# Kernel tuning notes

Measured on AMD Instinct MI355X. Metric: run time of the kernel, lower is better.

Reference implementation:

```python
import jax, jax.numpy as jnp
import numpy as np

E_LAMBDA = 1e-4


def _conv1d(x, w, b=None, pad=0):
    # x: (C, L) unbatched, w: (O, I, K)
    y = jax.lax.conv_general_dilated(
        x[None], w, window_strides=(1,), padding=[(pad, pad)],
        dimension_numbers=("NCH", "OIH", "NCH"))[0]
    if b is not None:
        y = y + b[:, None]
    return y


def _avg_pool2(x):
    # kernel 2 stride 2 along last axis; x: (C, L) -> (C, L//2)
    C, L = x.shape
    return x.reshape(C, L // 2, 2).mean(axis=-1)


def _simam(x):
    # x: (C, L); torch version runs on (1, C, L) so stats are global
    n = x.shape[0] * x.shape[1] - 1
    d = (x - x.mean()) ** 2
    y = d / (4.0 * (d.sum() / n + E_LAMBDA)) + 0.5
    return x + x * jax.nn.sigmoid(y)


def setup_inputs() -> dict:
    key = jax.random.key(0)
    ks = jax.random.split(key, 6)
    C, L = 2048, 4096  # L must equal 2*C for Tiss broadcast to be valid
    inp = jax.random.normal(ks[0], (C, L), dtype=jnp.float32)
    insum = jax.random.normal(ks[1], (C, L), dtype=jnp.float32)
    conv1_w = jax.random.normal(ks[2], (C, C, 3), dtype=jnp.float32) * (1.0 / np.sqrt(3 * C))
    fc_w = jax.random.normal(ks[3], (C, C, 1), dtype=jnp.float32) * (1.0 / np.sqrt(C))
    fc_b = jax.random.normal(ks[4], (C,), dtype=jnp.float32) * 0.01
    mix_w = jnp.array([-0.8], dtype=jnp.float32)
    return {"input": inp, "insum": insum, "conv1_w": conv1_w,
            "fc_w": fc_w, "fc_b": fc_b, "mix_w": mix_w}


def reference(input, insum, conv1_w, fc_w, fc_b, mix_w):
    x = _avg_pool2(input)        # (C, L/2)
    x_mfcc = _avg_pool2(insum)   # (C, L/2)

    input_new = _simam(input)
    insum_new = _simam(insum)

    x1 = _conv1d(x, conv1_w, pad=1)          # (C, L/2)
    x_mfcc1 = _conv1d(x_mfcc, conv1_w, pad=1)
    x2 = _conv1d(x, fc_w, fc_b, pad=0).T      # (L/2, C)
    x_mfcc2 = _conv1d(x_mfcc1, fc_w, fc_b, pad=0).T  # (L/2, C)

    out1 = jax.nn.sigmoid((x1 @ x_mfcc2).sum(axis=1))          # (C,)
    out2 = jax.nn.sigmoid((x_mfcc1.T @ x2.T).sum(axis=1))      # (L/2,) == (C,)

    mf = jax.nn.sigmoid(mix_w)                                  # (1,)
    out = out1 * mf + out2 * (1.0 - mf)                         # (C,)

    out = jax.nn.sigmoid(_conv1d(out[:, None], conv1_w, pad=1))  # (C, 1)

    input_insum = input_new * 0.6 + insum_new * 0.4             # (C, L)
    return input_insum * out
```

## Files before the change

kernel.cpp:

```cpp
#include <hip/hip_runtime.h>
#include <math.h>

#define C  2048
#define L  4096
#define L2 2048
#define CW3 6144

constexpr size_t OFF_RS_A = 0;
constexpr size_t OFF_RQ_A = 2048;
constexpr size_t OFF_RS_B = 4096;
constexpr size_t OFF_RQ_B = 6144;
constexpr size_t OFF_SCAL = 8192;
constexpr size_t OFF_CW   = 8208;
constexpr size_t OFF_G    = 10256;
constexpr size_t OFF_H    = 16400;
constexpr size_t OFF_V    = 22544;
constexpr size_t OFF_O2   = 24592;
constexpr size_t OFF_S    = 26640;
constexpr size_t OFF_U    = 28688;
constexpr size_t OFF_MIX  = 34832;

constexpr size_t PA_OFF = 0;
constexpr size_t PB_OFF = 4194304;

__device__ __forceinline__ float wredf(float v) {
#pragma unroll
  for (int o = 32; o; o >>= 1) v += __shfl_down(v, o, 64);
  return v;
}
__device__ __forceinline__ double wredd(double v) {
#pragma unroll
  for (int o = 32; o; o >>= 1) v += __shfl_down(v, o, 64);
  return v;
}
__device__ __forceinline__ float sigm(float x) { return 1.f / (1.f + expf(-x)); }
__device__ __forceinline__ float simam1(float x, float m, float cf) {
  float d = x - m;
  float y = d * d * cf + 0.5f;
  return x * (1.f + 1.f / (1.f + expf(-y)));
}

__global__ void w1(const float* __restrict__ A, const float* __restrict__ B,
                   const float* __restrict__ fc_w, float* __restrict__ ws,
                   float* __restrict__ dout) {
  int u = blockIdx.x;
  int tid = threadIdx.x;
  if (u < 4096) {
    __shared__ float sm[8];
    const float* src = (u < 2048) ? A : B;
    int row = u & 2047;
    const float4* p = (const float4*)(src + (size_t)row * L);
    float4* pool = (float4*)(dout + ((u < 2048) ? PA_OFF : PB_OFF) + (size_t)row * L2);
    float s = 0.f, q = 0.f;
#pragma unroll
    for (int i = tid; i < L2 / 4; i += 256) {
      float4 v0 = p[2 * i], v1 = p[2 * i + 1];
      s += ((v0.x + v0.y) + (v0.z + v0.w)) + ((v1.x + v1.y) + (v1.z + v1.w));
      q += (v0.x * v0.x + v0.y * v0.y) + (v0.z * v0.z + v0.w * v0.w) +
           (v1.x * v1.x + v1.y * v1.y) + (v1.z * v1.z + v1.w * v1.w);
      float4 pm;
      pm.x = (v0.x + v0.y) * 0.5f;
      pm.y = (v0.z + v0.w) * 0.5f;
      pm.z = (v1.x + v1.y) * 0.5f;
      pm.w = (v1.z + v1.w) * 0.5f;
      pool[i] = pm;
    }
    s = wredf(s); q = wredf(q);
    int lane = tid & 63, wv = tid >> 6;
    if (!lane) { sm[wv] = s; sm[4 + wv] = q; }
    __syncthreads();
    if (!tid) {
      float* rs = ws + ((u < 2048) ? OFF_RS_A : OFF_RS_B);
      float* rq = ws + ((u < 2048) ? OFF_RQ_A : OFF_RQ_B);
      rs[row] = sm[0] + sm[1] + sm[2] + sm[3];
      rq[row] = sm[4] + sm[5] + sm[6] + sm[7];
    }
  } else {
    int cb = u - 4096;
    int rg = cb >> 3;
    int col = (cb & 7) * 256 + tid;
    const float* p = fc_w + (size_t)rg * 64 * C + col;
    float acc = 0.f;
#pragma unroll 8
    for (int k = 0; k < 64; ++k) acc += p[(size_t)k * C];
    atomicAdd(ws + OFF_CW + col, acc);
  }
}

__global__ void w2(const float* __restrict__ fc_w, const float* __restrict__ fc_b,
                   float* __restrict__ ws) {
  int u = blockIdx.x, tid = threadIdx.x;
  int lane = tid & 63, wv = tid >> 6;
  if (u < 512) {
    __shared__ float sl[16];
    int r0 = u * 4;
    const float4* rx = (const float4*)(ws + OFF_RS_A);
    const float4* w4 = (const float4*)fc_w;
    float a0 = 0.f, a1 = 0.f, a2 = 0.f, a3 = 0.f;
#pragma unroll
    for (int i = tid; i < C / 4; i += 256) {
      float4 r = rx[i];
      float4 q0 = w4[(size_t)(r0 + 0) * 512 + i];
      float4 q1 = w4[(size_t)(r0 + 1) * 512 + i];
      float4 q2 = w4[(size_t)(r0 + 2) * 512 + i];
      float4 q3 = w4[(size_t)(r0 + 3) * 512 + i];
      a0 += q0.x * r.x + q0.y * r.y + q0.z * r.z + q0.w * r.w;
      a1 += q1.x * r.x + q1.y * r.y + q1.z * r.z + q1.w * r.w;
      a2 += q2.x * r.x + q2.y * r.y + q2.z * r.z + q2.w * r.w;
      a3 += q3.x * r.x + q3.y * r.y + q3.z * r.z + q3.w * r.w;
    }
    a0 = wredf(a0); a1 = wredf(a1); a2 = wredf(a2); a3 = wredf(a3);
    if (!lane) { sl[wv] = a0; sl[4 + wv] = a1; sl[8 + wv] = a2; sl[12 + wv] = a3; }
    __syncthreads();
    if (tid < 4) {
      float s_ = sl[tid * 4 + 0] + sl[tid * 4 + 1] + sl[tid * 4 + 2] + sl[tid * 4 + 3];
      ws[OFF_S + r0 + tid] = 0.5f * s_ + (float)L2 * fc_b[r0 + tid];
    }
  } else {
    __shared__ double sd[5];
    const float* arr = ws + (wv == 0 ? OFF_RS_A : wv == 1 ? OFF_RQ_A
                                                          : wv == 2 ? OFF_RS_B : OFF_RQ_B);
    double acc = 0.0, accb = 0.0;
    for (int i = lane; i < 2048; i += 64) {
      acc += (double)arr[i];
      if (wv == 0) accb += (double)fc_b[i];
    }
    acc = wredd(acc);
    if (wv == 0) accb = wredd(accb);
    if (!lane) { sd[wv] = acc; if (wv == 0) sd[4] = accb; }
    __syncthreads();
    if (!tid) {
      const double N = (double)C * (double)L, n = N - 1.0;
      double dA = sd[1] - sd[0] * sd[0] / N;
      double dB = sd[3] - sd[2] * sd[2] / N;
      float* sc = ws + OFF_SCAL;
      sc[0] = (float)(sd[0] / N);
      sc[1] = (float)(1.0 / (4.0 * (dA / n + 1e-4)));
      sc[2] = (float)(sd[2] / N);
      sc[3] = (float)(1.0 / (4.0 * (dB / n + 1e-4)));
      sc[4] = (float)sd[4];
    }
  }
}

__global__ void w3(const float* __restrict__ conv1_w, float* __restrict__ ws) {
  __shared__ float lcw[64], ls[64];
  int u = blockIdx.x;
  int tid = threadIdx.x;
  int cc = u % 24, rg = u / 24;
  int col = cc * 256 + tid;
  int i0 = rg * 64;
  if (tid < 64) {
    lcw[tid] = (ws + OFF_CW)[i0 + tid];
    ls[tid] = (ws + OFF_S)[i0 + tid];
  }
  __syncthreads();
  const float* base = conv1_w + (size_t)i0 * CW3 + col;
  float ag = 0.f, ah = 0.f;
#pragma unroll 8
  for (int k = 0; k < 64; ++k) {
    float wv = base[(size_t)k * CW3];
    ag += lcw[k] * wv;
    ah += ls[k] * wv;
  }
  atomicAdd(ws + OFF_G + col, ag);
  atomicAdd(ws + OFF_H + col, ah);
}

__global__ void w4(const float* __restrict__ dout, float* __restrict__ ws) {
  __shared__ float gs[96], hs[96];
  int u = blockIdx.x;
  int tid = threadIdx.x;
  int kb = u & 7, cg = u >> 3;
  int c0 = cg * 32;
  int k = kb * 256 + tid;
  int lane = tid & 63;
  if (tid < 96) gs[tid] = (ws + OFF_G)[c0 * 3 + tid];
  else if (tid >= 128 && tid < 224) hs[tid - 128] = (ws + OFF_H)[c0 * 3 + tid - 128];
  __syncthreads();
  float accv = 0.f, acco = 0.f;
#pragma unroll 4
  for (int c = 0; c < 32; ++c) {
    const float* row = dout + PB_OFF + (size_t)(c0 + c) * L2;
    float xc = row[k];
    float xl = __shfl_up(xc, 1, 64);
    float xr = __shfl_down(xc, 1, 64);
    if (lane == 0)  xl = (k > 0) ? row[k - 1] : 0.f;
    if (lane == 63) xr = (k < L2 - 1) ? row[k + 1] : 0.f;
    accv += gs[c * 3] * xl + gs[c * 3 + 1] * xc + gs[c * 3 + 2] * xr;
    acco += hs[c * 3] * xl + hs[c * 3 + 1] * xc + hs[c * 3 + 2] * xr;
  }
  atomicAdd(ws + OFF_V + k, accv);
  atomicAdd(ws + OFF_O2 + k, acco);
}

__global__ void w5(const float* __restrict__ dout, float* __restrict__ ws) {
  __shared__ float vsh[2050];
  __shared__ float s12[12];
  int u = blockIdx.x;
  int tid = threadIdx.x;
  float sb = (ws + OFF_SCAL)[4];
  if (tid == 0) { vsh[0] = 0.f; vsh[2049] = 0.f; }
  for (int j = tid; j < L2; j += 256) vsh[1 + j] = (ws + OFF_V)[j] + sb;
  __syncthreads();
  const float* prow = dout + PA_OFF + (size_t)u * L2;
  float a0 = 0.f, a1 = 0.f, a2 = 0.f;
#pragma unroll
  for (int j = tid; j < L2; j += 256) {
    float xm = prow[j];
    a0 += xm * vsh[j + 2];
    a1 += xm * vsh[j + 1];
    a2 += xm * vsh[j];
  }
  a0 = wredf(a0); a1 = wredf(a1); a2 = wredf(a2);
  int lane = tid & 63, wv = tid >> 6;
  if (!lane) { s12[wv] = a0; s12[4 + wv] = a1; s12[8 + wv] = a2; }
  __syncthreads();
  if (!tid) {
    (ws + OFF_U)[u * 3 + 0] = s12[0] + s12[1] + s12[2] + s12[3];
    (ws + OFF_U)[u * 3 + 1] = s12[4] + s12[5] + s12[6] + s12[7];
    (ws + OFF_U)[u * 3 + 2] = s12[8] + s12[9] + s12[10] + s12[11];
  }
}

__global__ void w6(const float* __restrict__ conv1_w, const float* __restrict__ mix_w,
                   float* __restrict__ ws) {
  __shared__ float sl[4];
  int u = blockIdx.x;
  int tid = threadIdx.x;
  const float4* w4p = (const float4*)(conv1_w + (size_t)u * CW3);
  const float4* u4 = (const float4*)(ws + OFF_U);
  float acc = 0.f;
#pragma unroll
  for (int m = tid; m < CW3 / 4; m += 256) {
    float4 wv = w4p[m], uv = u4[m];
    acc += wv.x * uv.x + wv.y * uv.y + wv.z * uv.z + wv.w * uv.w;
  }
  acc = wredf(acc);
  int lane = tid & 63, wv = tid >> 6;
  if (!lane) sl[wv] = acc;
  __syncthreads();
  if (!tid) {
    float mfv = sigm(mix_w[0]);
    float o1 = sigm(sl[0] + sl[1] + sl[2] + sl[3]);
    float o2 = sigm((ws + OFF_O2)[u]);
    (ws + OFF_MIX)[u] = o1 * mfv + o2 * (1.f - mfv);
  }
}

__global__ void w7(const float* __restrict__ input, const float* __restrict__ insum,
                   const float* __restrict__ conv1_w, float* __restrict__ out,
                   const float* __restrict__ ws) {
  __shared__ float sl[4];
  __shared__ float shov;
  int u = blockIdx.x;
  int tid = threadIdx.x;
  const float4* w4p = (const float4*)(conv1_w + (size_t)u * CW3);
  const float4* m4 = (const float4*)(ws + OFF_MIX);
  float acc = 0.f;
#pragma unroll
  for (int p = tid; p < 512; p += 256) {
    float4 f0 = w4p[3 * p], f1 = w4p[3 * p + 1], f2 = w4p[3 * p + 2];
    float4 m = m4[p];
    acc += f0.y * m.x + f1.x * m.y + f1.w * m.z + f2.z * m.w;
  }
  acc = wredf(acc);
  int lane = tid & 63, wv = tid >> 6;
  if (!lane) sl[wv] = acc;
  __syncthreads();
  if (!tid) shov = sigm(sl[0] + sl[1] + sl[2] + sl[3]);
  __syncthreads();
  float ovc = shov;
  const float* scal = ws + OFF_SCAL;
  float mA = scal[0], cA = scal[1], mB = scal[2], cB = scal[3];
  size_t base = (size_t)u * L;
  const float4* pa = (const float4*)(input + base);
  const float4* pb = (const float4*)(insum + base);
  float4* po = (float4*)(out + base);
#pragma unroll
  for (int i = tid; i < L / 4; i += 256) {
    float4 a = pa[i], b = pb[i], r;
    r.x = (simam1(a.x, mA, cA) * 0.6f + simam1(b.x, mB, cB) * 0.4f) * ovc;
    r.y = (simam1(a.y, mA, cA) * 0.6f + simam1(b.y, mB, cB) * 0.4f) * ovc;
    r.z = (simam1(a.z, mA, cA) * 0.6f + simam1(b.z, mB, cB) * 0.4f) * ovc;
    r.w = (simam1(a.w, mA, cA) * 0.6f + simam1(b.w, mB, cB) * 0.4f) * ovc;
    po[i] = r;
  }
}

extern "C" void kernel_launch(void* const* d_in, const int* in_sizes, int n_in,
                              void* d_out, int out_size, void* d_ws, size_t ws_size,
                              hipStream_t stream) {
  const float* input   = (const float*)d_in[0];
  const float* insum   = (const float*)d_in[1];
  const float* conv1_w = (const float*)d_in[2];
  const float* fc_w    = (const float*)d_in[3];
  const float* fc_b    = (const float*)d_in[4];
  const float* mix_w   = (const float*)d_in[5];
  float* out = (float*)d_out;
  float* ws  = (float*)d_ws;

  hipMemsetAsync((char*)d_ws + OFF_CW * 4, 0, 18432 * 4, stream);

  dim3 b(256);
  w1<<<4352, b, 0, stream>>>(input, insum, fc_w, ws, out);
  w2<<<513, b, 0, stream>>>(fc_w, fc_b, ws);
  w3<<<768, b, 0, stream>>>(conv1_w, ws);
  w4<<<512, b, 0, stream>>>(out, ws);
  w5<<<2048, b, 0, stream>>>(out, ws);
  w6<<<2048, b, 0, stream>>>(conv1_w, mix_w, ws);
  w7<<<2048, b, 0, stream>>>(input, insum, conv1_w, out, ws);
}
```

Measured before the change: 235.6 us.

## Fold workspace memset into w1, move fc_w column sums to w2, vectorize w3-w5

The separate hipMemsetAsync is removed; extra blocks in w1 now zero the accumulator region with float4 stores. The fc_w column-sum blocks move from w1 into w2, so they run alongside the small reductions there. w3, w4 and w5 switch to float4 loads, with each thread handling four columns (w3, w4) or each block handling two rows (w5), cutting grid sizes. The aim is to save a launch, shorten the long w1 grid and improve memory-load efficiency. The cost is more atomics per thread and fewer blocks, which may lower occupancy in w3 and w4.

```diff
diff --git a/kernel.cpp b/kernel.cpp
--- a/kernel.cpp
+++ b/kernel.cpp
@@ -41,8 +41,7 @@
 }
 
 __global__ void w1(const float* __restrict__ A, const float* __restrict__ B,
-                   const float* __restrict__ fc_w, float* __restrict__ ws,
-                   float* __restrict__ dout) {
+                   float* __restrict__ ws, float* __restrict__ dout) {
   int u = blockIdx.x;
   int tid = threadIdx.x;
   if (u < 4096) {
@@ -76,14 +75,9 @@
       rq[row] = sm[4] + sm[5] + sm[6] + sm[7];
     }
   } else {
-    int cb = u - 4096;
-    int rg = cb >> 3;
-    int col = (cb & 7) * 256 + tid;
-    const float* p = fc_w + (size_t)rg * 64 * C + col;
-    float acc = 0.f;
-#pragma unroll 8
-    for (int k = 0; k < 64; ++k) acc += p[(size_t)k * C];
-    atomicAdd(ws + OFF_CW + col, acc);
+    float4* wz = (float4*)(ws + OFF_CW);
+    int i = (u - 4096) * 256 + tid;
+    wz[i] = make_float4(0.f, 0.f, 0.f, 0.f);
   }
 }
 
@@ -116,7 +110,7 @@
       float s_ = sl[tid * 4 + 0] + sl[tid * 4 + 1] + sl[tid * 4 + 2] + sl[tid * 4 + 3];
       ws[OFF_S + r0 + tid] = 0.5f * s_ + (float)L2 * fc_b[r0 + tid];
     }
-  } else {
+  } else if (u == 512) {
     __shared__ double sd[5];
     const float* arr = ws + (wv == 0 ? OFF_RS_A : wv == 1 ? OFF_RQ_A
                                                           : wv == 2 ? OFF_RS_B : OFF_RQ_B);
@@ -140,6 +134,15 @@
       sc[3] = (float)(1.0 / (4.0 * (dB / n + 1e-4)));
       sc[4] = (float)sd[4];
     }
+  } else {
+    int cb = u - 513;
+    int rg = cb >> 3;
+    int col = (cb & 7) * 256 + tid;
+    const float* p = fc_w + (size_t)rg * 64 * C + col;
+    float acc = 0.f;
+#pragma unroll 8
+    for (int k = 0; k < 64; ++k) acc += p[(size_t)k * C];
+    atomicAdd(ws + OFF_CW + col, acc);
   }
 }
 
@@ -147,79 +150,113 @@
   __shared__ float lcw[64], ls[64];
   int u = blockIdx.x;
   int tid = threadIdx.x;
-  int cc = u % 24, rg = u / 24;
-  int col = cc * 256 + tid;
+  int cc = u % 6, rg = u / 6;
   int i0 = rg * 64;
+  int col4 = cc * 256 + tid;
   if (tid < 64) {
     lcw[tid] = (ws + OFF_CW)[i0 + tid];
     ls[tid] = (ws + OFF_S)[i0 + tid];
   }
   __syncthreads();
-  const float* base = conv1_w + (size_t)i0 * CW3 + col;
-  float ag = 0.f, ah = 0.f;
+  const float4* cv = (const float4*)conv1_w;
+  float4 g4 = {0.f, 0.f, 0.f, 0.f}, h4 = {0.f, 0.f, 0.f, 0.f};
 #pragma unroll 8
   for (int k = 0; k < 64; ++k) {
-    float wv = base[(size_t)k * CW3];
-    ag += lcw[k] * wv;
-    ah += ls[k] * wv;
-  }
-  atomicAdd(ws + OFF_G + col, ag);
-  atomicAdd(ws + OFF_H + col, ah);
+    float4 w = cv[(size_t)(i0 + k) * 1536 + col4];
+    float cwv = lcw[k], sv = ls[k];
+    g4.x += cwv * w.x; g4.y += cwv * w.y; g4.z += cwv * w.z; g4.w += cwv * w.w;
+    h4.x += sv * w.x;  h4.y += sv * w.y;  h4.z += sv * w.z;  h4.w += sv * w.w;
+  }
+  int col = col4 * 4;
+  atomicAdd(ws + OFF_G + col + 0, g4.x);
+  atomicAdd(ws + OFF_G + col + 1, g4.y);
+  atomicAdd(ws + OFF_G + col + 2, g4.z);
+  atomicAdd(ws + OFF_G + col + 3, g4.w);
+  atomicAdd(ws + OFF_H + col + 0, h4.x);
+  atomicAdd(ws + OFF_H + col + 1, h4.y);
+  atomicAdd(ws + OFF_H + col + 2, h4.z);
+  atomicAdd(ws + OFF_H + col + 3, h4.w);
 }
 
 __global__ void w4(const float* __restrict__ dout, float* __restrict__ ws) {
-  __shared__ float gs[96], hs[96];
-  int u = blockIdx.x;
-  int tid = threadIdx.x;
-  int kb = u & 7, cg = u >> 3;
-  int c0 = cg * 32;
-  int k = kb * 256 + tid;
+  __shared__ float gs[48], hs[48];
+  int u = blockIdx.x;
+  int tid = threadIdx.x;
+  int kb = u & 1, cg = u >> 1;
+  int c0 = cg * 16;
+  int q = kb * 256 + tid;
   int lane = tid & 63;
-  if (tid < 96) gs[tid] = (ws + OFF_G)[c0 * 3 + tid];
-  else if (tid >= 128 && tid < 224) hs[tid - 128] = (ws + OFF_H)[c0 * 3 + tid - 128];
-  __syncthreads();
-  float accv = 0.f, acco = 0.f;
+  if (tid < 48) gs[tid] = (ws + OFF_G)[c0 * 3 + tid];
+  else if (tid >= 64 && tid < 112) hs[tid - 64] = (ws + OFF_H)[c0 * 3 + tid - 64];
+  __syncthreads();
+  float4 accv = {0.f, 0.f, 0.f, 0.f}, acco = {0.f, 0.f, 0.f, 0.f};
 #pragma unroll 4
-  for (int c = 0; c < 32; ++c) {
+  for (int c = 0; c < 16; ++c) {
     const float* row = dout + PB_OFF + (size_t)(c0 + c) * L2;
-    float xc = row[k];
-    float xl = __shfl_up(xc, 1, 64);
-    float xr = __shfl_down(xc, 1, 64);
-    if (lane == 0)  xl = (k > 0) ? row[k - 1] : 0.f;
-    if (lane == 63) xr = (k < L2 - 1) ? row[k + 1] : 0.f;
-    accv += gs[c * 3] * xl + gs[c * 3 + 1] * xc + gs[c * 3 + 2] * xr;
-    acco += hs[c * 3] * xl + hs[c * 3 + 1] * xc + hs[c * 3 + 2] * xr;
-  }
-  atomicAdd(ws + OFF_V + k, accv);
-  atomicAdd(ws + OFF_O2 + k, acco);
+    float4 x = ((const float4*)row)[q];
+    float xlm = __shfl_up(x.w, 1, 64);
+    float xrp = __shfl_down(x.x, 1, 64);
+    if (lane == 0)  xlm = (q > 0) ? row[4 * q - 1] : 0.f;
+    if (lane == 63) xrp = (q < 511) ? row[4 * q + 4] : 0.f;
+    float g0 = gs[c * 3], g1 = gs[c * 3 + 1], g2 = gs[c * 3 + 2];
+    float h0 = hs[c * 3], h1 = hs[c * 3 + 1], h2 = hs[c * 3 + 2];
+    accv.x += g0 * xlm + g1 * x.x + g2 * x.y;
+    accv.y += g0 * x.x + g1 * x.y + g2 * x.z;
+    accv.z += g0 * x.y + g1 * x.z + g2 * x.w;
+    accv.w += g0 * x.z + g1 * x.w + g2 * xrp;
+    acco.x += h0 * xlm + h1 * x.x + h2 * x.y;
+    acco.y += h0 * x.x + h1 * x.y + h2 * x.z;
+    acco.z += h0 * x.y + h1 * x.z + h2 * x.w;
+    acco.w += h0 * x.z + h1 * x.w + h2 * xrp;
+  }
+  int k0 = 4 * q;
+  atomicAdd(ws + OFF_V + k0 + 0, accv.x);
+  atomicAdd(ws + OFF_V + k0 + 1, accv.y);
+  atomicAdd(ws + OFF_V + k0 + 2, accv.z);
+  atomicAdd(ws + OFF_V + k0 + 3, accv.w);
+  atomicAdd(ws + OFF_O2 + k0 + 0, acco.x);
+  atomicAdd(ws + OFF_O2 + k0 + 1, acco.y);
+  atomicAdd(ws + OFF_O2 + k0 + 2, acco.z);
+  atomicAdd(ws + OFF_O2 + k0 + 3, acco.w);
 }
 
 __global__ void w5(const float* __restrict__ dout, float* __restrict__ ws) {
-  __shared__ float vsh[2050];
+  __shared__ float4 vs4[512];
   __shared__ float s12[12];
-  int u = blockIdx.x;
-  int tid = threadIdx.x;
+  float* vs = (float*)vs4;
+  int u = blockIdx.x;
+  int tid = threadIdx.x;
+  int lane = tid & 63, wv = tid >> 6;
   float sb = (ws + OFF_SCAL)[4];
-  if (tid == 0) { vsh[0] = 0.f; vsh[2049] = 0.f; }
-  for (int j = tid; j < L2; j += 256) vsh[1 + j] = (ws + OFF_V)[j] + sb;
-  __syncthreads();
-  const float* prow = dout + PA_OFF + (size_t)u * L2;
-  float a0 = 0.f, a1 = 0.f, a2 = 0.f;
-#pragma unroll
-  for (int j = tid; j < L2; j += 256) {
-    float xm = prow[j];
-    a0 += xm * vsh[j + 2];
-    a1 += xm * vsh[j + 1];
-    a2 += xm * vsh[j];
-  }
-  a0 = wredf(a0); a1 = wredf(a1); a2 = wredf(a2);
-  int lane = tid & 63, wv = tid >> 6;
-  if (!lane) { s12[wv] = a0; s12[4 + wv] = a1; s12[8 + wv] = a2; }
-  __syncthreads();
-  if (!tid) {
-    (ws + OFF_U)[u * 3 + 0] = s12[0] + s12[1] + s12[2] + s12[3];
-    (ws + OFF_U)[u * 3 + 1] = s12[4] + s12[5] + s12[6] + s12[7];
-    (ws + OFF_U)[u * 3 + 2] = s12[8] + s12[9] + s12[10] + s12[11];
+  for (int j = tid; j < L2; j += 256) vs[j] = (ws + OFF_V)[j] + sb;
+  __syncthreads();
+#pragma unroll
+  for (int rr = 0; rr < 2; ++rr) {
+    int row = u * 2 + rr;
+    const float4* prow = (const float4*)(dout + PA_OFF + (size_t)row * L2);
+    float a0 = 0.f, a1 = 0.f, a2 = 0.f;
+#pragma unroll
+    for (int it = 0; it < 2; ++it) {
+      int i = it * 256 + tid;
+      float4 xm = prow[i];
+      float4 va = vs4[i];
+      float vm1 = __shfl_up(va.w, 1, 64);
+      float vp4 = __shfl_down(va.x, 1, 64);
+      if (lane == 0)  vm1 = (i > 0) ? vs[4 * i - 1] : 0.f;
+      if (lane == 63) vp4 = (i < 511) ? vs[4 * i + 4] : 0.f;
+      a1 += xm.x * va.x + xm.y * va.y + xm.z * va.z + xm.w * va.w;
+      a0 += xm.x * va.y + xm.y * va.z + xm.z * va.w + xm.w * vp4;
+      a2 += xm.x * vm1 + xm.y * va.x + xm.z * va.y + xm.w * va.z;
+    }
+    a0 = wredf(a0); a1 = wredf(a1); a2 = wredf(a2);
+    if (!lane) { s12[wv] = a0; s12[4 + wv] = a1; s12[8 + wv] = a2; }
+    __syncthreads();
+    if (!tid) {
+      (ws + OFF_U)[row * 3 + 0] = s12[0] + s12[1] + s12[2] + s12[3];
+      (ws + OFF_U)[row * 3 + 1] = s12[4] + s12[5] + s12[6] + s12[7];
+      (ws + OFF_U)[row * 3 + 2] = s12[8] + s12[9] + s12[10] + s12[11];
+    }
+    __syncthreads();
   }
 }
 
@@ -300,14 +337,12 @@
   float* out = (float*)d_out;
   float* ws  = (float*)d_ws;
 
-  hipMemsetAsync((char*)d_ws + OFF_CW * 4, 0, 18432 * 4, stream);
-
   dim3 b(256);
-  w1<<<4352, b, 0, stream>>>(input, insum, fc_w, ws, out);
-  w2<<<513, b, 0, stream>>>(fc_w, fc_b, ws);
-  w3<<<768, b, 0, stream>>>(conv1_w, ws);
-  w4<<<512, b, 0, stream>>>(out, ws);
-  w5<<<2048, b, 0, stream>>>(out, ws);
+  w1<<<4114, b, 0, stream>>>(input, insum, ws, out);
+  w2<<<769, b, 0, stream>>>(fc_w, fc_b, ws);
+  w3<<<192, b, 0, stream>>>(conv1_w, ws);
+  w4<<<256, b, 0, stream>>>(out, ws);
+  w5<<<1024, b, 0, stream>>>(out, ws);
   w6<<<2048, b, 0, stream>>>(conv1_w, mix_w, ws);
   w7<<<2048, b, 0, stream>>>(input, insum, conv1_w, out, ws);
 }
```

Measured after the change: 244.9 us. 3.9% more time.

## Drop pooled insum buffer and replace w3 atomics with partial-sum scratch

Applied to the files above, without the earlier changes.

The first kernel no longer writes the average-pooled copy of insum; w4 now recomputes the pooled values on the fly from insum with float2 loads. w3 writes per-row-group partial sums into scratch space in the output buffer instead of doing float atomics on the workspace, and w4 reduces those 32 partials itself. This removes a 16 MB write and its re-read, plus atomic contention, at the cost of w4 reading twice as many bytes from insum and doing a small extra reduction.

```diff
diff --git a/kernel.cpp b/kernel.cpp
--- a/kernel.cpp
+++ b/kernel.cpp
@@ -21,7 +21,8 @@
 constexpr size_t OFF_MIX  = 34832;
 
 constexpr size_t PA_OFF = 0;
-constexpr size_t PB_OFF = 4194304;
+constexpr size_t GP_OFF = 4194304;
+constexpr size_t HP_OFF = 4390912;
 
 __device__ __forceinline__ float wredf(float v) {
 #pragma unroll
@@ -50,7 +51,8 @@
     const float* src = (u < 2048) ? A : B;
     int row = u & 2047;
     const float4* p = (const float4*)(src + (size_t)row * L);
-    float4* pool = (float4*)(dout + ((u < 2048) ? PA_OFF : PB_OFF) + (size_t)row * L2);
+    float4* pool = (float4*)(dout + PA_OFF + (size_t)row * L2);
+    bool dopool = (u < 2048);
     float s = 0.f, q = 0.f;
 #pragma unroll
     for (int i = tid; i < L2 / 4; i += 256) {
@@ -58,12 +60,14 @@
       s += ((v0.x + v0.y) + (v0.z + v0.w)) + ((v1.x + v1.y) + (v1.z + v1.w));
       q += (v0.x * v0.x + v0.y * v0.y) + (v0.z * v0.z + v0.w * v0.w) +
            (v1.x * v1.x + v1.y * v1.y) + (v1.z * v1.z + v1.w * v1.w);
-      float4 pm;
-      pm.x = (v0.x + v0.y) * 0.5f;
-      pm.y = (v0.z + v0.w) * 0.5f;
-      pm.z = (v1.x + v1.y) * 0.5f;
-      pm.w = (v1.z + v1.w) * 0.5f;
-      pool[i] = pm;
+      if (dopool) {
+        float4 pm;
+        pm.x = (v0.x + v0.y) * 0.5f;
+        pm.y = (v0.z + v0.w) * 0.5f;
+        pm.z = (v1.x + v1.y) * 0.5f;
+        pm.w = (v1.z + v1.w) * 0.5f;
+        pool[i] = pm;
+      }
     }
     s = wredf(s); q = wredf(q);
     int lane = tid & 63, wv = tid >> 6;
@@ -143,7 +147,8 @@
   }
 }
 
-__global__ void w3(const float* __restrict__ conv1_w, float* __restrict__ ws) {
+__global__ void w3(const float* __restrict__ conv1_w, const float* __restrict__ ws,
+                   float* __restrict__ dout) {
   __shared__ float lcw[64], ls[64];
   int u = blockIdx.x;
   int tid = threadIdx.x;
@@ -163,11 +168,12 @@
     ag += lcw[k] * wv;
     ah += ls[k] * wv;
   }
-  atomicAdd(ws + OFF_G + col, ag);
-  atomicAdd(ws + OFF_H + col, ah);
-}
-
-__global__ void w4(const float* __restrict__ dout, float* __restrict__ ws) {
+  dout[GP_OFF + (size_t)rg * CW3 + col] = ag;
+  dout[HP_OFF + (size_t)rg * CW3 + col] = ah;
+}
+
+__global__ void w4(const float* __restrict__ insum, const float* __restrict__ scr,
+                   float* __restrict__ ws) {
   __shared__ float gs[96], hs[96];
   int u = blockIdx.x;
   int tid = threadIdx.x;
@@ -175,18 +181,36 @@
   int c0 = cg * 32;
   int k = kb * 256 + tid;
   int lane = tid & 63;
-  if (tid < 96) gs[tid] = (ws + OFF_G)[c0 * 3 + tid];
-  else if (tid >= 128 && tid < 224) hs[tid - 128] = (ws + OFF_H)[c0 * 3 + tid - 128];
+  if (tid < 96) {
+    const float* base = scr + GP_OFF + (size_t)c0 * 3 + tid;
+    float a = 0.f;
+#pragma unroll 8
+    for (int g = 0; g < 32; ++g) a += base[(size_t)g * CW3];
+    gs[tid] = a;
+  } else if (tid >= 128 && tid < 224) {
+    const float* base = scr + HP_OFF + (size_t)c0 * 3 + (tid - 128);
+    float a = 0.f;
+#pragma unroll 8
+    for (int g = 0; g < 32; ++g) a += base[(size_t)g * CW3];
+    hs[tid - 128] = a;
+  }
   __syncthreads();
   float accv = 0.f, acco = 0.f;
 #pragma unroll 4
   for (int c = 0; c < 32; ++c) {
-    const float* row = dout + PB_OFF + (size_t)(c0 + c) * L2;
-    float xc = row[k];
+    const float* row = insum + (size_t)(c0 + c) * L;
+    float2 fm = *(const float2*)(row + 2 * k);
+    float xc = 0.5f * (fm.x + fm.y);
     float xl = __shfl_up(xc, 1, 64);
     float xr = __shfl_down(xc, 1, 64);
-    if (lane == 0)  xl = (k > 0) ? row[k - 1] : 0.f;
-    if (lane == 63) xr = (k < L2 - 1) ? row[k + 1] : 0.f;
+    if (lane == 0) {
+      xl = 0.f;
+      if (k > 0) { float2 f = *(const float2*)(row + 2 * k - 2); xl = 0.5f * (f.x + f.y); }
+    }
+    if (lane == 63) {
+      xr = 0.f;
+      if (k < L2 - 1) { float2 f = *(const float2*)(row + 2 * k + 2); xr = 0.5f * (f.x + f.y); }
+    }
     accv += gs[c * 3] * xl + gs[c * 3 + 1] * xc + gs[c * 3 + 2] * xr;
     acco += hs[c * 3] * xl + hs[c * 3 + 1] * xc + hs[c * 3 + 2] * xr;
   }
@@ -305,8 +329,8 @@
   dim3 b(256);
   w1<<<4352, b, 0, stream>>>(input, insum, fc_w, ws, out);
   w2<<<513, b, 0, stream>>>(fc_w, fc_b, ws);
-  w3<<<768, b, 0, stream>>>(conv1_w, ws);
-  w4<<<512, b, 0, stream>>>(out, ws);
+  w3<<<768, b, 0, stream>>>(conv1_w, ws, out);
+  w4<<<512, b, 0, stream>>>(insum, out, ws);
   w5<<<2048, b, 0, stream>>>(out, ws);
   w6<<<2048, b, 0, stream>>>(conv1_w, mix_w, ws);
   w7<<<2048, b, 0, stream>>>(input, insum, conv1_w, out, ws);
```

Measured after the change: 249.0 us. 5.7% more time.
